# Kernel tuning notes

Measured on AMD Instinct MI355X. Metric: run time of the kernel, lower is better.

The kernel has to match this reference:

```python
import jax, jax.numpy as jnp
import numpy as np

B, NUM_CLASSES, H, W, CF = 2, 19, 64, 64, 256
TOPK_IDX = 20  # hard-coded in the torch source: sorted descending value at index 20


def _cosine(x):
    # x: [B, N, D] -> clamped cosine affinity [B, N, N]
    xn = x / (jnp.linalg.norm(x, axis=2, keepdims=True) + 1e-9)
    return jnp.maximum(jnp.einsum('bnd,bmd->bnm', xn, xn), 0.0)


def _conv1x1(x, w, b):
    # x: [B, C, H, W], w: [O, C], b: [O]
    return jnp.einsum('bchw,oc->bohw', x, w) + b[None, :, None, None]


def setup_inputs() -> dict:
    key = jax.random.key(0)
    ks = jax.random.split(key, 12)
    s_c = (2.0 / NUM_CLASSES) ** 0.5  # kaiming fan_in scale for 1x1 conv
    s_f = (2.0 / CF) ** 0.5
    return {
        'pred': jax.random.normal(ks[0], (B, NUM_CLASSES, H, W), jnp.float32),
        'feat': jax.random.normal(ks[1], (B, CF, H, W), jnp.float32),
        'w_cls1': jax.random.normal(ks[2], (NUM_CLASSES, NUM_CLASSES), jnp.float32) * s_c,
        'b_cls1': jnp.zeros((NUM_CLASSES,), jnp.float32),
        'w_cls2': jax.random.normal(ks[3], (NUM_CLASSES, NUM_CLASSES), jnp.float32) * s_c,
        'b_cls2': jnp.zeros((NUM_CLASSES,), jnp.float32),
        'w_pro1': jax.random.normal(ks[4], (CF, CF), jnp.float32) * s_f,
        'b_pro1': jnp.zeros((CF,), jnp.float32),
        'w_pro2': jax.random.normal(ks[5], (CF, CF), jnp.float32) * s_f,
        'b_pro2': jnp.zeros((CF,), jnp.float32),
        'class_weight': jnp.ones((NUM_CLASSES,), jnp.float32),
    }


def reference(pred, feat, w_cls1, b_cls1, w_cls2, b_cls2,
              w_pro1, b_pro1, w_pro2, b_pro2, class_weight):
    bsz, c, h, w = feat.shape
    C = pred.shape[1]
    N = h * w
    feat_flat = feat.reshape(bsz, c, N).transpose(0, 2, 1)  # [B, N, 256]

    # --- no_grad block 1: confidence mask + top-k sparsified cosine affinity ---
    prob = jax.nn.softmax(pred, axis=1)
    p_prob = prob.max(axis=1)      # [B, H, W]
    p_max = prob.argmax(axis=1)    # [B, H, W]
    cwm = class_weight / (class_weight.max() + 1e-10) * 0.95
    mask = ((p_prob >= 0.95) | (p_prob >= cwm[p_max])).astype(jnp.float32)
    mask = jax.lax.stop_gradient(mask.reshape(bsz, N, 1))  # broadcast over classes

    aff1 = _cosine(feat_flat)                                # [B, N, N]
    thr = -jnp.sort(-aff1, axis=-1)[:, :, TOPK_IDX:TOPK_IDX + 1]  # per-row 21st largest
    aff1 = jnp.where(aff1 < thr, 0.0, aff1)
    aff1 = jax.lax.stop_gradient(aff1 + aff1.transpose(0, 2, 1))

    # --- degree-normalized propagation of predictions ---
    pred_flat = pred.reshape(bsz, C, N).transpose(0, 2, 1)   # [B, N, C]
    d1 = (aff1.sum(-1) + 1e-10) ** -0.5                      # D^{-1/2}
    aff1n = d1[:, :, None] * aff1 * d1[:, None, :]           # D^{-1/2} A D^{-1/2}
    p2 = jnp.einsum('bnm,bmc->bnc', aff1n, pred_flat)
    p3 = (0.8 * p2 + 0.2 * pred_flat) * (1.0 - mask) + (0.2 * p2 + 0.8 * pred_flat) * mask
    pred2 = p3.transpose(0, 2, 1).reshape(bsz, C, h, w)
    pred_out = _conv1x1(_conv1x1(pred2, w_cls1, b_cls1), w_cls2, b_cls2)

    # --- no_grad block 2: class-consistency-masked affinity over refined softmax ---
    oh = jax.nn.one_hot(p_max, C, dtype=jnp.float32)         # [B, H, W, C]
    # faithful to torch: permute(0,2,3,1) on the already-[B,H,W,C] one-hot, then flat view
    oh = jnp.transpose(oh, (0, 2, 3, 1)).reshape(bsz, -1, C)
    sp = jax.nn.softmax(pred_out, axis=1).reshape(bsz, C, N).transpose(0, 2, 1)
    aff_f = _cosine(sp)
    aff_f = jnp.where(_cosine(oh) == 0.0, 0.0, aff_f)
    d2 = (aff_f.sum(-1) + 1e-10) ** -0.5
    aff_fn = jax.lax.stop_gradient(d2[:, :, None] * aff_f * d2[:, None, :])

    # --- propagate features and project ---
    new_feat = jnp.einsum('bnm,bmc->bnc', aff_fn, feat_flat)
    new_feat = new_feat.transpose(0, 2, 1).reshape(bsz, c, h, w)
    feat_out = _conv1x1(jax.nn.relu(_conv1x1(new_feat, w_pro1, b_pro1)), w_pro2, b_pro2)
    return pred_out, feat_out
```

## Files before the change

### kernel.cpp

```cpp
#include <hip/hip_runtime.h>

#define NN 4096
#define DD 256
#define CC 19
#define BB 2
#define KSPLIT 4

typedef __attribute__((ext_vector_type(8))) short bf16x8;
typedef _Float16 f16x8 __attribute__((ext_vector_type(8)));
typedef __attribute__((ext_vector_type(4))) float f32x4;

#define GLL16(gp, lp) __builtin_amdgcn_global_load_lds( \
    (const __attribute__((address_space(1))) unsigned int*)(gp), \
    (__attribute__((address_space(3))) unsigned int*)(lp), 16, 0, 0)

__device__ inline unsigned short f2b(float f) {
  unsigned int u = __float_as_uint(f);
  return (unsigned short)((u + 0x7FFFu + ((u >> 16) & 1u)) >> 16);
}
__device__ inline float b2f(unsigned short h) {
  return __uint_as_float(((unsigned int)h) << 16);
}
__device__ inline unsigned int pack2(float a, float b) {
  return (unsigned int)f2b(a) | ((unsigned int)f2b(b) << 16);
}
__device__ inline void split16(float x, unsigned short& h, unsigned short& l) {
  _Float16 hh = (_Float16)x;
  float hf = (float)hh;
  _Float16 ll = (_Float16)((x - hf) * 2048.0f);
  h = *reinterpret_cast<unsigned short*>(&hh);
  l = *reinterpret_cast<unsigned short*>(&ll);
}

__global__ __launch_bounds__(256) void k_prep(const float* __restrict__ pred,
                                              const float* __restrict__ cw,
                                              const float* __restrict__ feat,
                                              float* __restrict__ maskb,
                                              unsigned int* __restrict__ ohbits,
                                              unsigned short* __restrict__ xh,
                                              unsigned short* __restrict__ xl) {
  int g = blockIdx.x * 256 + threadIdx.x;
  int b = g >> 12, n = g & (NN - 1);
  {
    const float* p = pred + (size_t)b * CC * NN + n;
    float v[CC];
    float mx = -1e30f; int am = 0;
#pragma unroll
    for (int c = 0; c < CC; ++c) {
      float t = p[(size_t)c * NN];
      v[c] = t;
      if (t > mx) { mx = t; am = c; }
    }
    float s = 0.f;
#pragma unroll
    for (int c = 0; c < CC; ++c) s += expf(v[c] - mx);
    float pprob = 1.f / s;
    float cmax = 0.f;
#pragma unroll
    for (int c = 0; c < CC; ++c) cmax = fmaxf(cmax, cw[c]);
    float cwm = cw[am] / (cmax + 1e-10f) * 0.95f;
    maskb[g] = (pprob >= 0.95f || pprob >= cwm) ? 1.f : 0.f;
    int h = n >> 6, w = n & 63;
    int L = w * (CC * 64) + am * 64 + h;
    atomicOr(&ohbits[b * NN + L / CC], 1u << (L % CC));
  }
  {
    const float* f = feat + (size_t)b * DD * NN + n;
    float s = 0.f;
    for (int d = 0; d < DD; ++d) { float t = f[(size_t)d * NN]; s += t * t; }
    float r = 1.f / (sqrtf(s) + 1e-9f);
    size_t ob = ((size_t)b * NN + n) * DD;
    for (int d = 0; d < DD; d += 4) {
      ushort4 oh, ol;
      split16(f[(size_t)d * NN] * r, oh.x, ol.x);
      split16(f[(size_t)(d + 1) * NN] * r, oh.y, ol.y);
      split16(f[(size_t)(d + 2) * NN] * r, oh.z, ol.z);
      split16(f[(size_t)(d + 3) * NN] * r, oh.w, ol.w);
      *reinterpret_cast<ushort4*>(&xh[ob + d]) = oh;
      *reinterpret_cast<ushort4*>(&xl[ob + d]) = ol;
    }
  }
}

__global__ __launch_bounds__(256, 2) void k_gram1(const unsigned short* __restrict__ xh,
                                                  const unsigned short* __restrict__ xl,
                                                  float* __restrict__ M) {
  int L = blockIdx.x;
  int b = blockIdx.y;
  int I = 0;
  while (L >= 32 - I) { L -= 32 - I; ++I; }
  int J = I + L;
  int i0 = I * 128, j0 = J * 128;
  float* Mb = M + (size_t)b * NN * NN;
  const unsigned short* XH = xh + (size_t)b * NN * DD;
  const unsigned short* XL = xl + (size_t)b * NN * DD;
  __shared__ unsigned short stage[2][4][128][32];
  int t = threadIdx.x;
  int wave = t >> 6, lane = t & 63;
  int wr = (wave & 1) * 64, wc = (wave >> 1) * 64;
  int lrow = lane & 15, quad = lane >> 4;
  int sel = (lrow >> 1) & 3;
  f32x4 accH[4][4] = {}, accL[4][4] = {};
  const unsigned short* src = (wave == 0) ? XH + (size_t)i0 * DD
                             : (wave == 1) ? XL + (size_t)i0 * DD
                             : (wave == 2) ? XH + (size_t)j0 * DD
                                           : XL + (size_t)j0 * DD;
  int srow = lane >> 2;
  int spart = (lane & 3) ^ ((lane >> 3) & 3);
#pragma unroll
  for (int e = 0; e < 8; ++e)
    GLL16(&src[(size_t)(e * 16 + srow) * DD + spart * 8], &stage[0][wave][e * 16][0]);
  __syncthreads();
  int cur = 0;
  for (int k0 = 0; k0 < DD; k0 += 32) {
    if (k0 + 32 < DD) {
#pragma unroll
      for (int e = 0; e < 8; ++e)
        GLL16(&src[(size_t)(e * 16 + srow) * DD + k0 + 32 + spart * 8],
              &stage[cur ^ 1][wave][e * 16][0]);
    }
    f16x8 ah[4], al[4], bh[4], bl[4];
#pragma unroll
    for (int i = 0; i < 4; ++i) {
      int ra = wr + i * 16 + lrow;
      int rb = wc + i * 16 + lrow;
      int sl = (quad ^ sel) * 8;
      ah[i] = *reinterpret_cast<const f16x8*>(&stage[cur][0][ra][sl]);
      al[i] = *reinterpret_cast<const f16x8*>(&stage[cur][1][ra][sl]);
      bh[i] = *reinterpret_cast<const f16x8*>(&stage[cur][2][rb][sl]);
      bl[i] = *reinterpret_cast<const f16x8*>(&stage[cur][3][rb][sl]);
    }
#pragma unroll
    for (int i = 0; i < 4; ++i) {
#pragma unroll
      for (int j = 0; j < 4; ++j) {
        accH[i][j] = __builtin_amdgcn_mfma_f32_16x16x32_f16(ah[i], bh[j], accH[i][j], 0, 0, 0);
        accL[i][j] = __builtin_amdgcn_mfma_f32_16x16x32_f16(ah[i], bl[j], accL[i][j], 0, 0, 0);
        accL[i][j] = __builtin_amdgcn_mfma_f32_16x16x32_f16(al[i], bh[j], accL[i][j], 0, 0, 0);
      }
    }
    __syncthreads();
    cur ^= 1;
  }
#pragma unroll
  for (int i = 0; i < 4; ++i)
#pragma unroll
    for (int j = 0; j < 4; ++j)
#pragma unroll
      for (int reg = 0; reg < 4; ++reg)
        accH[i][j][reg] = fmaxf(accH[i][j][reg] + accL[i][j][reg] * 4.8828125e-4f, 0.f);
  float* buf = (float*)stage;
  int rr = t >> 4, cc = t & 15;
  for (int half = 0; half < 2; ++half) {
    __syncthreads();
    if ((wr >> 6) == half) {
#pragma unroll
      for (int i = 0; i < 4; ++i)
#pragma unroll
        for (int j = 0; j < 4; ++j)
#pragma unroll
          for (int reg = 0; reg < 4; ++reg)
            buf[(i * 16 + quad * 4 + reg) * 132 + wc + j * 16 + lrow] = accH[i][j][reg];
    }
    __syncthreads();
#pragma unroll
    for (int i = 0; i < 4; ++i) {
      int row = rr + i * 16;
#pragma unroll
      for (int q = 0; q < 2; ++q) {
        int col = cc * 4 + q * 64;
        *reinterpret_cast<float4*>(&Mb[(size_t)(i0 + half * 64 + row) * NN + j0 + col]) =
            *reinterpret_cast<float4*>(&buf[row * 132 + col]);
      }
    }
  }
  if (I != J) {
    for (int half = 0; half < 2; ++half) {
      __syncthreads();
      if ((wc >> 6) == half) {
#pragma unroll
        for (int i = 0; i < 4; ++i)
#pragma unroll
          for (int j = 0; j < 4; ++j)
#pragma unroll
            for (int reg = 0; reg < 4; ++reg)
              buf[(j * 16 + lrow) * 132 + wr + i * 16 + quad * 4 + reg] = accH[i][j][reg];
      }
      __syncthreads();
#pragma unroll
      for (int i = 0; i < 4; ++i) {
        int row = rr + i * 16;
#pragma unroll
        for (int q = 0; q < 2; ++q) {
          int col = cc * 4 + q * 64;
          *reinterpret_cast<float4*>(&Mb[(size_t)(j0 + half * 64 + row) * NN + i0 + col]) =
              *reinterpret_cast<float4*>(&buf[row * 132 + col]);
        }
      }
    }
  }
}

__global__ __launch_bounds__(256, 2) void k_topk(const float* __restrict__ M,
                                                 float* __restrict__ thr) {
  __shared__ unsigned int cbuf[4][64];
  int b = blockIdx.y;
  int wave = threadIdx.x >> 6, lane = threadIdx.x & 63;
  int n = blockIdx.x * 4 + wave;
  const float* row = M + (size_t)b * NN * NN + (size_t)n * NN;
  uint4 v[16];
#pragma unroll
  for (int e = 0; e < 16; ++e) {
    unsigned long long addr = (unsigned long long)(row + lane * 4 + e * 256);
    asm volatile("global_load_dwordx4 %0, %1, off" : "=v"(v[e]) : "v"(addr));
  }
  asm volatile("s_waitcnt vmcnt(0)" ::: "memory");
  __builtin_amdgcn_sched_barrier(0);
  unsigned int mx = 0u;
#pragma unroll
  for (int e = 0; e < 16; ++e) {
    unsigned int a = v[e].x > v[e].y ? v[e].x : v[e].y;
    unsigned int c2 = v[e].z > v[e].w ? v[e].z : v[e].w;
    a = a > c2 ? a : c2;
    mx = mx > a ? mx : a;
  }
  unsigned int lo = 0u, hi = 0x3FC00000u;
  while (lo < hi) {
    unsigned int mid = lo + ((hi - lo + 1) >> 1);
    if (__popcll(__ballot(mx >= mid)) >= 21) lo = mid; else hi = mid - 1;
  }
  unsigned int s = lo;
  unsigned int base = 0;
  unsigned long long ltmask = (1ull << lane) - 1ull;
#pragma unroll
  for (int e = 0; e < 16; ++e) {
#pragma unroll
    for (int q = 0; q < 4; ++q) {
      unsigned int val = (q == 0) ? v[e].x : (q == 1) ? v[e].y : (q == 2) ? v[e].z : v[e].w;
      unsigned long long mk = __ballot(val >= s);
      if (mk) {
        unsigned int pos = base + (unsigned int)__popcll(mk & ltmask);
        if (val >= s && pos < 64u) cbuf[wave][pos] = val;
        base += (unsigned int)__popcll(mk);
      }
    }
  }
  asm volatile("s_waitcnt lgkmcnt(0)" ::: "memory");
  __builtin_amdgcn_sched_barrier(0);
  unsigned int t = s;
  if (base <= 64u) {
    unsigned int cand = (lane < (int)base) ? cbuf[wave][lane] : 0u;
    lo = s; hi = 0x3FC00000u;
    while (lo < hi) {
      unsigned int mid = lo + ((hi - lo + 1) >> 1);
      if (__popcll(__ballot(cand >= mid)) >= 21) lo = mid; else hi = mid - 1;
    }
    t = lo;
  }
  {
    unsigned int t1 = t + 1u;
    int c1 = 0, c2 = 0;
#pragma unroll
    for (int e = 0; e < 16; ++e) {
      c1 += (int)__popcll(__ballot(v[e].x >= t));
      c1 += (int)__popcll(__ballot(v[e].y >= t));
      c1 += (int)__popcll(__ballot(v[e].z >= t));
      c1 += (int)__popcll(__ballot(v[e].w >= t));
      c2 += (int)__popcll(__ballot(v[e].x >= t1));
      c2 += (int)__popcll(__ballot(v[e].y >= t1));
      c2 += (int)__popcll(__ballot(v[e].z >= t1));
      c2 += (int)__popcll(__ballot(v[e].w >= t1));
    }
    if (!(c1 >= 21 && c2 < 21)) {
      lo = 0u; hi = 0x40000000u;
      while (lo < hi) {
        unsigned int mid = lo + ((hi - lo + 1) >> 1);
        int c = 0;
#pragma unroll
        for (int e = 0; e < 16; ++e) {
          c += (int)__popcll(__ballot(v[e].x >= mid));
          c += (int)__popcll(__ballot(v[e].y >= mid));
          c += (int)__popcll(__ballot(v[e].z >= mid));
          c += (int)__popcll(__ballot(v[e].w >= mid));
        }
        if (c >= 21) lo = mid; else hi = mid - 1;
      }
      t = lo;
    }
  }
  if (lane == 0) thr[b * NN + n] = __uint_as_float(t);
}

__global__ __launch_bounds__(256) void k_symm(float* __restrict__ M, const float* __restrict__ thr,
                                              float* __restrict__ dsum) {
  int L = blockIdx.x;
  int b = blockIdx.y;
  int I = 0;
  while (L >= 64 - I) { L -= 64 - I; ++I; }
  int J = I + L;
  float* Mb = M + (size_t)b * NN * NN;
  unsigned short* Mus = (unsigned short*)Mb;
  const float* th = thr + b * NN;
  __shared__ float A[64][65];
  int t = threadIdx.x;
  int i0 = I * 64, j0 = J * 64;
  float areg[16];
#pragma unroll
  for (int e = 0; e < 16; ++e) {
    int lin = t + e * 256;
    int i = lin >> 6, j = lin & 63;
    areg[e] = Mb[(size_t)(i0 + i) * NN + j0 + j];
  }
#pragma unroll
  for (int e = 0; e < 16; ++e) {
    int lin = t + e * 256;
    int i = lin >> 6, j = lin & 63;
    float a = areg[e];
    float v = a * ((a >= th[i0 + i] ? 1.f : 0.f) + (a >= th[j0 + j] ? 1.f : 0.f));
    A[i][j] = v;
  }
  __syncthreads();
  {
    int i = t >> 2, seg = (t & 3) * 16;
    float v[16];
#pragma unroll
    for (int q = 0; q < 4; ++q)
      *reinterpret_cast<float4*>(&v[q * 4]) = *reinterpret_cast<float4*>(&A[i][seg + q * 4]);
    unsigned int pk[8];
#pragma unroll
    for (int q = 0; q < 8; ++q) pk[q] = pack2(v[2 * q], v[2 * q + 1]);
    size_t ub = 2 * (size_t)(i0 + i) * NN + 2 * (size_t)j0 + seg;
    *reinterpret_cast<int4*>(&Mus[ub])     = *reinterpret_cast<int4*>(&pk[0]);
    *reinterpret_cast<int4*>(&Mus[ub + 8]) = *reinterpret_cast<int4*>(&pk[4]);
  }
  if (I != J) {
    int j = t >> 2, seg = (t & 3) * 16;
    float v[16];
#pragma unroll
    for (int e = 0; e < 16; ++e) v[e] = A[seg + e][j];
    unsigned int pk[8];
#pragma unroll
    for (int q = 0; q < 8; ++q) pk[q] = pack2(v[2 * q], v[2 * q + 1]);
    size_t ub = 2 * (size_t)(j0 + j) * NN + 2 * (size_t)i0 + seg;
    *reinterpret_cast<int4*>(&Mus[ub])     = *reinterpret_cast<int4*>(&pk[0]);
    *reinterpret_cast<int4*>(&Mus[ub + 8]) = *reinterpret_cast<int4*>(&pk[4]);
  }
  if (t < 64) {
    float s = 0.f;
#pragma unroll
    for (int j = 0; j < 64; ++j) s += A[t][j];
    atomicAdd(&dsum[b * NN + i0 + t], s);
  } else if (t < 128 && I != J) {
    int j = t - 64;
    float s = 0.f;
#pragma unroll
    for (int i = 0; i < 64; ++i) s += A[i][j];
    atomicAdd(&dsum[b * NN + j0 + j], s);
  }
}

__global__ void k_make_yb(const float* __restrict__ pred, const float* __restrict__ d1,
                          unsigned short* __restrict__ ybh) {
  int g = blockIdx.x * 256 + threadIdx.x;
  int idx = g * 4;
  int b = idx / (32 * NN);
  int c = (idx / NN) & 31;
  int n = idx & (NN - 1);
  ushort4 o = make_ushort4(0, 0, 0, 0);
  if (c < CC) {
    float4 p = *reinterpret_cast<const float4*>(&pred[((size_t)b * CC + c) * NN + n]);
    const float* dd = d1 + b * NN + n;
    o.x = f2b(p.x * (1.f / sqrtf(dd[0] + 1e-10f)));
    o.y = f2b(p.y * (1.f / sqrtf(dd[1] + 1e-10f)));
    o.z = f2b(p.z * (1.f / sqrtf(dd[2] + 1e-10f)));
    o.w = f2b(p.w * (1.f / sqrtf(dd[3] + 1e-10f)));
  }
  *reinterpret_cast<ushort4*>(&ybh[idx]) = o;
}

__global__ __launch_bounds__(256, 2) void k_p2_mfma(
    const float* __restrict__ M, const unsigned short* __restrict__ ybh,
    const float* __restrict__ d1, float* __restrict__ p2b) {
  int b = blockIdx.y;
  int n0 = blockIdx.x * 64;
  const unsigned short* Mus = (const unsigned short*)(M + (size_t)b * NN * NN);
  const unsigned short* Y = ybh + (size_t)b * 32 * NN;
  __shared__ unsigned short As2[2][64][64];
  __shared__ unsigned short Ys2[2][32][64];
  int t = threadIdx.x;
  int wave = t >> 6, lane = t & 63;
  int wn = (wave & 1) * 32;
  int wc = (wave >> 1) * 16;
  int lrow = lane & 15, quad = lane >> 4;
  f32x4 acc[2] = {{0.f,0.f,0.f,0.f},{0.f,0.f,0.f,0.f}};
  int lr3 = lane >> 3;
  int srow = wave * 8 + lr3;
  int spart = (lane & 7) ^ lr3;
#pragma unroll
  for (int e = 0; e < 2; ++e)
    GLL16(&Mus[2 * (size_t)(n0 + e * 32 + srow) * NN + spart * 8],
          &As2[0][e * 32 + wave * 8][0]);
  GLL16(&Y[(size_t)srow * NN + spart * 8], &Ys2[0][wave * 8][0]);
  __syncthreads();
  int cur = 0;
  for (int m0 = 0; m0 < NN; m0 += 64) {
    if (m0 + 64 < NN) {
#pragma unroll
      for (int e = 0; e < 2; ++e)
        GLL16(&Mus[2 * (size_t)(n0 + e * 32 + srow) * NN + 2 * (size_t)(m0 + 64) + spart * 8],
              &As2[cur ^ 1][e * 32 + wave * 8][0]);
      GLL16(&Y[(size_t)srow * NN + m0 + 64 + spart * 8], &Ys2[cur ^ 1][wave * 8][0]);
    }
#pragma unroll
    for (int kc = 0; kc < 2; ++kc) {
      int sl = ((kc * 4 + quad) ^ (lrow & 7)) * 8;
      bf16x8 bfr = *reinterpret_cast<const bf16x8*>(&Ys2[cur][wc + lrow][sl]);
#pragma unroll
      for (int i = 0; i < 2; ++i) {
        bf16x8 af = *reinterpret_cast<const bf16x8*>(&As2[cur][wn + i * 16 + lrow][sl]);
        acc[i] = __builtin_amdgcn_mfma_f32_16x16x32_bf16(af, bfr, acc[i], 0, 0, 0);
      }
    }
    __syncthreads();
    cur ^= 1;
  }
  int c = wc + lrow;
  if (c < CC) {
#pragma unroll
    for (int i = 0; i < 2; ++i) {
#pragma unroll
      for (int reg = 0; reg < 4; ++reg) {
        int n = n0 + wn + i * 16 + quad * 4 + reg;
        float dv = 1.f / sqrtf(d1[b * NN + n] + 1e-10f);
        p2b[((size_t)b * NN + n) * CC + c] = dv * acc[i][reg];
      }
    }
  }
}

__global__ __launch_bounds__(256) void k_pred_head(const float* __restrict__ pred,
    const float* __restrict__ p2b, const float* __restrict__ maskb,
    const float* __restrict__ w1, const float* __restrict__ b1,
    const float* __restrict__ w2, const float* __restrict__ b2,
    float* __restrict__ out, float* __restrict__ spnT) {
  __shared__ float sw1[CC * CC], sw2[CC * CC], sb1[CC], sb2[CC];
  int t = threadIdx.x;
  for (int i = t; i < CC * CC; i += 256) { sw1[i] = w1[i]; sw2[i] = w2[i]; }
  if (t < CC) { sb1[t] = b1[t]; sb2[t] = b2[t]; }
  __syncthreads();
  int g = blockIdx.x * 256 + t;
  int b = g >> 12, n = g & (NN - 1);
  float m = maskb[g];
  float ca = (m > 0.5f) ? 0.2f : 0.8f;
  float cb = (m > 0.5f) ? 0.8f : 0.2f;
  const float* P = pred + (size_t)b * CC * NN + n;
  const float* Q = p2b + (size_t)g * CC;
  float p3[CC];
#pragma unroll
  for (int c = 0; c < CC; ++c) p3[c] = ca * Q[c] + cb * P[(size_t)c * NN];
  float midv[CC];
#pragma unroll
  for (int o = 0; o < CC; ++o) {
    float s = sb1[o];
#pragma unroll
    for (int c = 0; c < CC; ++c) s += sw1[o * CC + c] * p3[c];
    midv[o] = s;
  }
  float ov[CC];
  float mx = -1e30f;
#pragma unroll
  for (int o = 0; o < CC; ++o) {
    float s = sb2[o];
#pragma unroll
    for (int c = 0; c < CC; ++c) s += sw2[o * CC + c] * midv[c];
    ov[o] = s;
    out[(size_t)b * CC * NN + (size_t)o * NN + n] = s;
    mx = fmaxf(mx, s);
  }
  float se = 0.f;
  float e[CC];
#pragma unroll
  for (int o = 0; o < CC; ++o) { e[o] = expf(ov[o] - mx); se += e[o]; }
  float inv = 1.f / se;
  float nrm = 0.f;
#pragma unroll
  for (int o = 0; o < CC; ++o) { float sp = e[o] * inv; e[o] = sp; nrm += sp * sp; }
  float rn = 1.f / (sqrtf(nrm) + 1e-9f);
#pragma unroll
  for (int o = 0; o < CC; ++o) spnT[(size_t)b * CC * NN + (size_t)o * NN + n] = e[o] * rn;
}

__global__ __launch_bounds__(256) void k_gram2(const float* __restrict__ spnT,
    const unsigned int* __restrict__ bits, unsigned short* __restrict__ Mh,
    float* __restrict__ d2) {
  int L = blockIdx.x;
  int b = blockIdx.y;
  int I = 0;
  while (L >= 64 - I) { L -= 64 - I; ++I; }
  int J = I + L;
  const float* X = spnT + (size_t)b * CC * NN;
  unsigned short* Mb = Mh + (size_t)b * NN * NN;
  __shared__ float sA[CC][64], sB[CC][64];
  __shared__ unsigned int bI[64], bJ[64];
  __shared__ float tr[64][65];
  int t = threadIdx.x;
  int r = t >> 4, c = t & 15;
  int i0 = I * 64, j0 = J * 64;
  for (int e = t; e < CC * 64; e += 256) {
    int k = e >> 6, col = e & 63;
    sA[k][col] = X[(size_t)k * NN + i0 + col];
    sB[k][col] = X[(size_t)k * NN + j0 + col];
  }
  if (t < 64) bI[t] = bits[b * NN + i0 + t];
  else if (t < 128) bJ[t - 64] = bits[b * NN + j0 + t - 64];
  __syncthreads();
  float acc[4][4] = {};
#pragma unroll
  for (int k = 0; k < CC; ++k) {
    float av[4], bv[4];
#pragma unroll
    for (int i = 0; i < 4; ++i) av[i] = sA[k][r * 4 + i];
#pragma unroll
    for (int j = 0; j < 4; ++j) bv[j] = sB[k][c * 4 + j];
#pragma unroll
    for (int i = 0; i < 4; ++i) {
#pragma unroll
      for (int j = 0; j < 4; ++j) acc[i][j] += av[i] * bv[j];
    }
  }
  float rs[4];
#pragma unroll
  for (int i = 0; i < 4; ++i) {
#pragma unroll
    for (int j = 0; j < 4; ++j) {
      bool keep = (bI[r * 4 + i] & bJ[c * 4 + j]) != 0u;
      acc[i][j] = keep ? fmaxf(acc[i][j], 0.f) : 0.f;
      acc[i][j] = b2f(f2b(acc[i][j]));
    }
    ushort4 v;
    v.x = f2b(acc[i][0]); v.y = f2b(acc[i][1]); v.z = f2b(acc[i][2]); v.w = f2b(acc[i][3]);
    *reinterpret_cast<ushort4*>(&Mb[(size_t)(i0 + r * 4 + i) * NN + j0 + c * 4]) = v;
    rs[i] = acc[i][0] + acc[i][1] + acc[i][2] + acc[i][3];
  }
#pragma unroll
  for (int m = 1; m < 16; m <<= 1) {
#pragma unroll
    for (int i = 0; i < 4; ++i) rs[i] += __shfl_xor(rs[i], m);
  }
  if ((t & 15) == 0) {
#pragma unroll
    for (int i = 0; i < 4; ++i) atomicAdd(&d2[b * NN + i0 + r * 4 + i], rs[i]);
  }
  if (I != J) {
#pragma unroll
    for (int i = 0; i < 4; ++i) {
#pragma unroll
      for (int j = 0; j < 4; ++j) tr[r * 4 + i][c * 4 + j] = acc[i][j];
    }
    __syncthreads();
#pragma unroll
    for (int e = 0; e < 16; ++e) {
      int lin = t + e * 256;
      int jr = lin >> 6, ic = lin & 63;
      Mb[(size_t)(j0 + jr) * NN + i0 + ic] = f2b(tr[ic][jr]);
    }
    if (t < 64) {
      float s = 0.f;
#pragma unroll
      for (int i = 0; i < 64; ++i) s += tr[i][t];
      atomicAdd(&d2[b * NN + j0 + t], s);
    }
  }
}

__global__ void k_make_z(const float* __restrict__ feat, const float* __restrict__ d2,
                         unsigned short* __restrict__ zb) {
  int g = blockIdx.x * 256 + threadIdx.x;
  int idx = g * 4;
  int b = idx / (DD * NN);
  int m = idx & (NN - 1);
  float4 f = *reinterpret_cast<const float4*>(&feat[idx]);
  const float* dd = d2 + b * NN + m;
  ushort4 o;
  o.x = f2b(f.x * (1.f / sqrtf(dd[0] + 1e-10f)));
  o.y = f2b(f.y * (1.f / sqrtf(dd[1] + 1e-10f)));
  o.z = f2b(f.z * (1.f / sqrtf(dd[2] + 1e-10f)));
  o.w = f2b(f.w * (1.f / sqrtf(dd[3] + 1e-10f)));
  *reinterpret_cast<ushort4*>(&zb[idx]) = o;
}

__global__ void k_prep_w(const float* __restrict__ w1, const float* __restrict__ w2,
                         unsigned short* __restrict__ wb1, unsigned short* __restrict__ wb2) {
  int g = blockIdx.x * 256 + threadIdx.x;
  wb1[g] = f2b(w1[g]);
  wb2[g] = f2b(w2[g]);
}

__global__ __launch_bounds__(256, 2) void k_newfeat_mfma(
    const unsigned short* __restrict__ Mh, const unsigned short* __restrict__ zb,
    float* __restrict__ nfp) {
  int zz = blockIdx.z;
  int b = zz / KSPLIT, ks = zz % KSPLIT;
  int nblk = blockIdx.x;
  int dblk = blockIdx.y;
  const int KLEN = NN / KSPLIT;
  const unsigned short* A = zb + (size_t)b * DD * NN + (size_t)(dblk * 64) * NN + ks * KLEN;
  const unsigned short* Bm = Mh + (size_t)b * NN * NN + (size_t)(nblk * 64) * NN + ks * KLEN;
  __shared__ unsigned short As[2][64][64];
  __shared__ unsigned short Bs[2][64][64];
  int t = threadIdx.x;
  int wave = t >> 6, lane = t & 63;
  int wd = (wave & 1) * 32, wn = (wave >> 1) * 32;
  int lrow = lane & 15, quad = lane >> 4;
  f32x4 acc[2][2] = {{{0.f,0.f,0.f,0.f},{0.f,0.f,0.f,0.f}},{{0.f,0.f,0.f,0.f},{0.f,0.f,0.f,0.f}}};
  int lr3 = lane >> 3;
  int srow = wave * 8 + lr3;
  int spart = (lane & 7) ^ lr3;
#pragma unroll
  for (int e = 0; e < 2; ++e) {
    GLL16(&A [(size_t)(e * 32 + srow) * NN + spart * 8], &As[0][e * 32 + wave * 8][0]);
    GLL16(&Bm[(size_t)(e * 32 + srow) * NN + spart * 8], &Bs[0][e * 32 + wave * 8][0]);
  }
  __syncthreads();
  int cur = 0;
  for (int m0 = 0; m0 < KLEN; m0 += 64) {
    if (m0 + 64 < KLEN) {
#pragma unroll
      for (int e = 0; e < 2; ++e) {
        GLL16(&A [(size_t)(e * 32 + srow) * NN + m0 + 64 + spart * 8],
              &As[cur ^ 1][e * 32 + wave * 8][0]);
        GLL16(&Bm[(size_t)(e * 32 + srow) * NN + m0 + 64 + spart * 8],
              &Bs[cur ^ 1][e * 32 + wave * 8][0]);
      }
    }
#pragma unroll
    for (int kc = 0; kc < 2; ++kc) {
      int sl = ((kc * 4 + quad) ^ (lrow & 7)) * 8;
      bf16x8 af[2], bfr[2];
#pragma unroll
      for (int i = 0; i < 2; ++i) {
        af[i]  = *reinterpret_cast<const bf16x8*>(&As[cur][wd + i * 16 + lrow][sl]);
        bfr[i] = *reinterpret_cast<const bf16x8*>(&Bs[cur][wn + i * 16 + lrow][sl]);
      }
#pragma unroll
      for (int i = 0; i < 2; ++i)
#pragma unroll
        for (int j = 0; j < 2; ++j)
          acc[i][j] = __builtin_amdgcn_mfma_f32_16x16x32_bf16(af[i], bfr[j], acc[i][j], 0, 0, 0);
    }
    __syncthreads();
    cur ^= 1;
  }
#pragma unroll
  for (int j = 0; j < 2; ++j) {
    int n = nblk * 64 + wn + j * 16 + lrow;
#pragma unroll
    for (int i = 0; i < 2; ++i) {
      int d = dblk * 64 + wd + i * 16 + quad * 4;
      float4 v = make_float4(acc[i][j].x, acc[i][j].y, acc[i][j].z, acc[i][j].w);
      *reinterpret_cast<float4*>(&nfp[((size_t)zz * NN + n) * DD + d]) = v;
    }
  }
}

__global__ void k_nf_reduce(const float* __restrict__ nfp, const float* __restrict__ d2,
                            unsigned short* __restrict__ nfh) {
  int g = blockIdx.x * 256 + threadIdx.x;
  int idx = g * 4;
  int b = idx / (NN * DD);
  int n = (idx / DD) & (NN - 1);
  size_t base = (size_t)idx + (size_t)b * (KSPLIT - 1) * NN * DD;
  float4 s = make_float4(0.f, 0.f, 0.f, 0.f);
#pragma unroll
  for (int ks = 0; ks < KSPLIT; ++ks) {
    float4 v = *reinterpret_cast<const float4*>(&nfp[base + (size_t)ks * NN * DD]);
    s.x += v.x; s.y += v.y; s.z += v.z; s.w += v.w;
  }
  float sc = 1.f / sqrtf(d2[b * NN + n] + 1e-10f);
  ushort4 o;
  o.x = f2b(s.x * sc); o.y = f2b(s.y * sc); o.z = f2b(s.z * sc); o.w = f2b(s.w * sc);
  *reinterpret_cast<ushort4*>(&nfh[idx]) = o;
}

__global__ __launch_bounds__(256) void k_conv1_mfma(
    const unsigned short* __restrict__ nfh, const unsigned short* __restrict__ wb1,
    const float* __restrict__ b1, unsigned short* __restrict__ midh) {
  int b = blockIdx.z;
  int nblk = blockIdx.x;
  int oblk = blockIdx.y;
  int n0 = nblk * 64, o0 = oblk * 64;
  __shared__ unsigned short As[64][72];
  __shared__ unsigned short Bs[64][72];
  int t = threadIdx.x;
  int wave = t >> 6, lane = t & 63;
  int wn = (wave & 1) * 32, wo = (wave >> 1) * 32;
  int lrow = lane & 15, quad = lane >> 4;
  f32x4 acc[2][2] = {{{0.f,0.f,0.f,0.f},{0.f,0.f,0.f,0.f}},{{0.f,0.f,0.f,0.f},{0.f,0.f,0.f,0.f}}};
  int sr = t >> 3, sc = (t & 7) * 8;
  for (int d0 = 0; d0 < DD; d0 += 64) {
#pragma unroll
    for (int e = 0; e < 2; ++e) {
      int rr = sr + e * 32;
      *reinterpret_cast<int4*>(&As[rr][sc]) =
          *reinterpret_cast<const int4*>(&nfh[((size_t)b * NN + n0 + rr) * DD + d0 + sc]);
      *reinterpret_cast<int4*>(&Bs[rr][sc]) =
          *reinterpret_cast<const int4*>(&wb1[(size_t)(o0 + rr) * DD + d0 + sc]);
    }
    __syncthreads();
#pragma unroll
    for (int kc = 0; kc < 2; ++kc) {
      int ko = kc * 32 + quad * 8;
      bf16x8 af[2], bfr[2];
#pragma unroll
      for (int i = 0; i < 2; ++i) {
        af[i]  = *reinterpret_cast<const bf16x8*>(&As[wn + i * 16 + lrow][ko]);
        bfr[i] = *reinterpret_cast<const bf16x8*>(&Bs[wo + i * 16 + lrow][ko]);
      }
#pragma unroll
      for (int i = 0; i < 2; ++i)
#pragma unroll
        for (int j = 0; j < 2; ++j)
          acc[i][j] = __builtin_amdgcn_mfma_f32_16x16x32_bf16(af[i], bfr[j], acc[i][j], 0, 0, 0);
    }
    __syncthreads();
  }
#pragma unroll
  for (int j = 0; j < 2; ++j) {
    int o = o0 + wo + j * 16 + lrow;
    float bias = b1[o];
#pragma unroll
    for (int i = 0; i < 2; ++i) {
      int nb = n0 + wn + i * 16 + quad * 4;
      ushort4 v;
      v.x = f2b(fmaxf(acc[i][j].x + bias, 0.f));
      v.y = f2b(fmaxf(acc[i][j].y + bias, 0.f));
      v.z = f2b(fmaxf(acc[i][j].z + bias, 0.f));
      v.w = f2b(fmaxf(acc[i][j].w + bias, 0.f));
      *reinterpret_cast<ushort4*>(&midh[((size_t)b * DD + o) * NN + nb]) = v;
    }
  }
}

__global__ __launch_bounds__(256) void k_conv2_mfma(
    const unsigned short* __restrict__ midh, const unsigned short* __restrict__ wb2,
    const float* __restrict__ b2, float* __restrict__ outp) {
  int b = blockIdx.z;
  int nblk = blockIdx.x;
  int oblk = blockIdx.y;
  int n0 = nblk * 64, o0 = oblk * 64;
  __shared__ unsigned short As[64][72];
  __shared__ unsigned short Bs[64][72];
  int t = threadIdx.x;
  int wave = t >> 6, lane = t & 63;
  int wn = (wave & 1) * 32, wo = (wave >> 1) * 32;
  int lrow = lane & 15, quad = lane >> 4;
  f32x4 acc[2][2] = {{{0.f,0.f,0.f,0.f},{0.f,0.f,0.f,0.f}},{{0.f,0.f,0.f,0.f},{0.f,0.f,0.f,0.f}}};
  int sr = t >> 3, sc = (t & 7) * 8;
  for (int d0 = 0; d0 < DD; d0 += 64) {
#pragma unroll
    for (int e = 0; e < 2; ++e) {
      int rr = sr + e * 32;
      *reinterpret_cast<int4*>(&Bs[rr][sc]) =
          *reinterpret_cast<const int4*>(&wb2[(size_t)(o0 + rr) * DD + d0 + sc]);
      unsigned short v[8];
      *reinterpret_cast<int4*>(v) =
          *reinterpret_cast<const int4*>(&midh[((size_t)b * DD + d0 + rr) * NN + n0 + sc]);
#pragma unroll
      for (int j = 0; j < 8; ++j) As[sc + j][rr] = v[j];
    }
    __syncthreads();
#pragma unroll
    for (int kc = 0; kc < 2; ++kc) {
      int ko = kc * 32 + quad * 8;
      bf16x8 af[2], bfr[2];
#pragma unroll
      for (int i = 0; i < 2; ++i) {
        af[i]  = *reinterpret_cast<const bf16x8*>(&As[wn + i * 16 + lrow][ko]);
        bfr[i] = *reinterpret_cast<const bf16x8*>(&Bs[wo + i * 16 + lrow][ko]);
      }
#pragma unroll
      for (int i = 0; i < 2; ++i)
#pragma unroll
        for (int j = 0; j < 2; ++j)
          acc[i][j] = __builtin_amdgcn_mfma_f32_16x16x32_bf16(af[i], bfr[j], acc[i][j], 0, 0, 0);
    }
    __syncthreads();
  }
#pragma unroll
  for (int j = 0; j < 2; ++j) {
    int o = o0 + wo + j * 16 + lrow;
    float bias = b2[o];
#pragma unroll
    for (int i = 0; i < 2; ++i) {
      int nb = n0 + wn + i * 16 + quad * 4;
      float4 v = make_float4(acc[i][j].x + bias, acc[i][j].y + bias,
                             acc[i][j].z + bias, acc[i][j].w + bias);
      *reinterpret_cast<float4*>(&outp[((size_t)b * DD + o) * NN + nb]) = v;
    }
  }
}

extern "C" void kernel_launch(void* const* d_in, const int* in_sizes, int n_in,
                              void* d_out, int out_size, void* d_ws, size_t ws_size,
                              hipStream_t stream) {
  (void)in_sizes; (void)n_in; (void)out_size; (void)ws_size;
  const float* pred   = (const float*)d_in[0];
  const float* feat   = (const float*)d_in[1];
  const float* w_cls1 = (const float*)d_in[2];
  const float* b_cls1 = (const float*)d_in[3];
  const float* w_cls2 = (const float*)d_in[4];
  const float* b_cls2 = (const float*)d_in[5];
  const float* w_pro1 = (const float*)d_in[6];
  const float* b_pro1 = (const float*)d_in[7];
  const float* w_pro2 = (const float*)d_in[8];
  const float* b_pro2 = (const float*)d_in[9];
  const float* cw     = (const float*)d_in[10];
  float* out = (float*)d_out;

  float* Mbuf = (float*)d_ws;
  float* spnT = Mbuf + (size_t)BB * NN * NN;
  float* p2b  = spnT + (size_t)BB * CC * NN;
  float* thr  = p2b + (size_t)BB * NN * CC;
  float* dsum = thr + BB * NN;
  float* d2s  = dsum + BB * NN;
  float* maskb = d2s + BB * NN;
  unsigned int* ohbits = (unsigned int*)(maskb + BB * NN);
  unsigned short* xh   = (unsigned short*)(ohbits + BB * NN);
  unsigned short* xl   = xh + (size_t)BB * NN * DD;
  unsigned short* nfh  = xl + (size_t)BB * NN * DD;
  unsigned short* midh = nfh + (size_t)BB * NN * DD;
  unsigned short* zb   = midh + (size_t)BB * DD * NN;
  unsigned short* wb1  = zb + (size_t)BB * DD * NN;
  unsigned short* wb2  = wb1 + (size_t)DD * DD;
  unsigned short* ybh  = wb2 + (size_t)DD * DD;
  unsigned short* Mh   = (unsigned short*)Mbuf;
  float* nfp = (float*)(Mh + (size_t)BB * NN * NN);

  hipMemsetAsync(dsum, 0, sizeof(float) * 2 * BB * NN, stream);
  hipMemsetAsync(ohbits, 0, sizeof(unsigned int) * BB * NN, stream);

  k_prep<<<BB * NN / 256, 256, 0, stream>>>(pred, cw, feat, maskb, ohbits, xh, xl);
  k_gram1<<<dim3(528, BB), 256, 0, stream>>>(xh, xl, Mbuf);
  k_topk<<<dim3(NN / 4, BB), 256, 0, stream>>>(Mbuf, thr);
  k_symm<<<dim3(2080, BB), 256, 0, stream>>>(Mbuf, thr, dsum);
  k_make_yb<<<BB * 32 * NN / 4 / 256, 256, 0, stream>>>(pred, dsum, ybh);
  k_p2_mfma<<<dim3(NN / 64, BB), 256, 0, stream>>>(Mbuf, ybh, dsum, p2b);
  k_pred_head<<<BB * NN / 256, 256, 0, stream>>>(pred, p2b, maskb, w_cls1, b_cls1,
                                                 w_cls2, b_cls2, out, spnT);
  k_gram2<<<dim3(2080, BB), 256, 0, stream>>>(spnT, ohbits, Mh, d2s);
  k_make_z<<<BB * DD * NN / 4 / 256, 256, 0, stream>>>(feat, d2s, zb);
  k_prep_w<<<DD * DD / 256, 256, 0, stream>>>(w_pro1, w_pro2, wb1, wb2);
  k_newfeat_mfma<<<dim3(64, 4, BB * KSPLIT), 256, 0, stream>>>(Mh, zb, nfp);
  k_nf_reduce<<<BB * NN * DD / 4 / 256, 256, 0, stream>>>(nfp, d2s, nfh);
  k_conv1_mfma<<<dim3(64, 4, BB), 256, 0, stream>>>(nfh, wb1, b_pro1, midh);
  k_conv2_mfma<<<dim3(64, 4, BB), 256, 0, stream>>>(midh, wb2, b_pro2,
                                                    out + (size_t)BB * CC * NN);
}
```

Before: 372.0 us.

## Compute second affinity Gram with bf16 MFMA from packed padded softmax rows

The pred head now writes the normalized softmax as bf16 rows padded to 32 channels instead of fp32 channel-major. The second Gram kernel loads those rows straight into LDS with global_load_lds and computes the 64x64 tile with 16x16x32 bf16 MFMA, replacing the scalar FMA loop. It stages the masked result in a bf16 LDS tile so the direct tile is written with wide row stores, and it takes row and column sums from that tile. Rounding the inputs to bf16 changes the affinity values slightly compared with the fp32 dot products.

New measurement: 332.4 us. -10.7%, faster.

```diff
diff --git a/kernel.cpp b/kernel.cpp
--- a/kernel.cpp
+++ b/kernel.cpp
@@ -442,7 +442,7 @@
     const float* __restrict__ p2b, const float* __restrict__ maskb,
     const float* __restrict__ w1, const float* __restrict__ b1,
     const float* __restrict__ w2, const float* __restrict__ b2,
-    float* __restrict__ out, float* __restrict__ spnT) {
+    float* __restrict__ out, unsigned short* __restrict__ spnP) {
   __shared__ float sw1[CC * CC], sw2[CC * CC], sb1[CC], sb2[CC];
   int t = threadIdx.x;
   for (int i = t; i < CC * CC; i += 256) { sw1[i] = w1[i]; sw2[i] = w2[i]; }
@@ -486,11 +486,18 @@
 #pragma unroll
   for (int o = 0; o < CC; ++o) { float sp = e[o] * inv; e[o] = sp; nrm += sp * sp; }
   float rn = 1.f / (sqrtf(nrm) + 1e-9f);
-#pragma unroll
-  for (int o = 0; o < CC; ++o) spnT[(size_t)b * CC * NN + (size_t)o * NN + n] = e[o] * rn;
-}
-
-__global__ __launch_bounds__(256) void k_gram2(const float* __restrict__ spnT,
+  unsigned short sp[32];
+#pragma unroll
+  for (int o = 0; o < CC; ++o) sp[o] = f2b(e[o] * rn);
+#pragma unroll
+  for (int o = CC; o < 32; ++o) sp[o] = 0;
+  unsigned short* dst = spnP + (size_t)g * 32;
+#pragma unroll
+  for (int q = 0; q < 4; ++q)
+    *reinterpret_cast<int4*>(&dst[q * 8]) = *reinterpret_cast<int4*>(&sp[q * 8]);
+}
+
+__global__ __launch_bounds__(256) void k_gram2(const unsigned short* __restrict__ spnP,
     const unsigned int* __restrict__ bits, unsigned short* __restrict__ Mh,
     float* __restrict__ d2) {
   int L = blockIdx.x;
@@ -498,78 +505,81 @@
   int I = 0;
   while (L >= 64 - I) { L -= 64 - I; ++I; }
   int J = I + L;
-  const float* X = spnT + (size_t)b * CC * NN;
+  const unsigned short* X = spnP + (size_t)b * NN * 32;
   unsigned short* Mb = Mh + (size_t)b * NN * NN;
-  __shared__ float sA[CC][64], sB[CC][64];
+  __shared__ unsigned short As[64][32], Bs[64][32];
+  __shared__ unsigned short tr[64][66];
   __shared__ unsigned int bI[64], bJ[64];
-  __shared__ float tr[64][65];
   int t = threadIdx.x;
-  int r = t >> 4, c = t & 15;
+  int wave = t >> 6, lane = t & 63;
+  int lrow = lane & 15, quad = lane >> 4;
   int i0 = I * 64, j0 = J * 64;
-  for (int e = t; e < CC * 64; e += 256) {
-    int k = e >> 6, col = e & 63;
-    sA[k][col] = X[(size_t)k * NN + i0 + col];
-    sB[k][col] = X[(size_t)k * NN + j0 + col];
-  }
+  int srow = wave * 16 + (lane >> 2);
+  int spart = (lane & 3) ^ ((lane >> 3) & 3);
+  GLL16(&X[(size_t)(i0 + srow) * 32 + spart * 8], &As[wave * 16][0]);
+  GLL16(&X[(size_t)(j0 + srow) * 32 + spart * 8], &Bs[wave * 16][0]);
   if (t < 64) bI[t] = bits[b * NN + i0 + t];
   else if (t < 128) bJ[t - 64] = bits[b * NN + j0 + t - 64];
   __syncthreads();
-  float acc[4][4] = {};
-#pragma unroll
-  for (int k = 0; k < CC; ++k) {
-    float av[4], bv[4];
-#pragma unroll
-    for (int i = 0; i < 4; ++i) av[i] = sA[k][r * 4 + i];
-#pragma unroll
-    for (int j = 0; j < 4; ++j) bv[j] = sB[k][c * 4 + j];
-#pragma unroll
-    for (int i = 0; i < 4; ++i) {
-#pragma unroll
-      for (int j = 0; j < 4; ++j) acc[i][j] += av[i] * bv[j];
-    }
-  }
-  float rs[4];
-#pragma unroll
-  for (int i = 0; i < 4; ++i) {
-#pragma unroll
-    for (int j = 0; j < 4; ++j) {
-      bool keep = (bI[r * 4 + i] & bJ[c * 4 + j]) != 0u;
-      acc[i][j] = keep ? fmaxf(acc[i][j], 0.f) : 0.f;
-      acc[i][j] = b2f(f2b(acc[i][j]));
-    }
-    ushort4 v;
-    v.x = f2b(acc[i][0]); v.y = f2b(acc[i][1]); v.z = f2b(acc[i][2]); v.w = f2b(acc[i][3]);
-    *reinterpret_cast<ushort4*>(&Mb[(size_t)(i0 + r * 4 + i) * NN + j0 + c * 4]) = v;
-    rs[i] = acc[i][0] + acc[i][1] + acc[i][2] + acc[i][3];
-  }
-#pragma unroll
-  for (int m = 1; m < 16; m <<= 1) {
-#pragma unroll
-    for (int i = 0; i < 4; ++i) rs[i] += __shfl_xor(rs[i], m);
-  }
-  if ((t & 15) == 0) {
-#pragma unroll
-    for (int i = 0; i < 4; ++i) atomicAdd(&d2[b * NN + i0 + r * 4 + i], rs[i]);
+  int wi = wave & 1, wj = wave >> 1;
+  int sl = (quad ^ ((lrow >> 1) & 3)) * 8;
+  bf16x8 af[2], bfr[2];
+#pragma unroll
+  for (int i = 0; i < 2; ++i) {
+    af[i]  = *reinterpret_cast<const bf16x8*>(&As[wi * 32 + i * 16 + lrow][sl]);
+    bfr[i] = *reinterpret_cast<const bf16x8*>(&Bs[wj * 32 + i * 16 + lrow][sl]);
+  }
+  f32x4 acc[2][2] = {{{0.f,0.f,0.f,0.f},{0.f,0.f,0.f,0.f}},{{0.f,0.f,0.f,0.f},{0.f,0.f,0.f,0.f}}};
+#pragma unroll
+  for (int i = 0; i < 2; ++i)
+#pragma unroll
+    for (int j = 0; j < 2; ++j)
+      acc[i][j] = __builtin_amdgcn_mfma_f32_16x16x32_bf16(af[i], bfr[j], acc[i][j], 0, 0, 0);
+#pragma unroll
+  for (int i = 0; i < 2; ++i) {
+#pragma unroll
+    for (int j = 0; j < 2; ++j) {
+#pragma unroll
+      for (int reg = 0; reg < 4; ++reg) {
+        int row = wi * 32 + i * 16 + quad * 4 + reg;
+        int col = wj * 32 + j * 16 + lrow;
+        bool keep = (bI[row] & bJ[col]) != 0u;
+        float v = keep ? fmaxf(acc[i][j][reg], 0.f) : 0.f;
+        tr[row][col] = f2b(v);
+      }
+    }
+  }
+  __syncthreads();
+  {
+    int row = t >> 2, seg = (t & 3) * 16;
+    unsigned int w[8];
+#pragma unroll
+    for (int k = 0; k < 8; ++k)
+      w[k] = *reinterpret_cast<const unsigned int*>(&tr[row][seg + 2 * k]);
+    *reinterpret_cast<int4*>(&Mb[(size_t)(i0 + row) * NN + j0 + seg])     =
+        *reinterpret_cast<int4*>(&w[0]);
+    *reinterpret_cast<int4*>(&Mb[(size_t)(i0 + row) * NN + j0 + seg + 8]) =
+        *reinterpret_cast<int4*>(&w[4]);
   }
   if (I != J) {
-#pragma unroll
-    for (int i = 0; i < 4; ++i) {
-#pragma unroll
-      for (int j = 0; j < 4; ++j) tr[r * 4 + i][c * 4 + j] = acc[i][j];
-    }
-    __syncthreads();
 #pragma unroll
     for (int e = 0; e < 16; ++e) {
       int lin = t + e * 256;
       int jr = lin >> 6, ic = lin & 63;
-      Mb[(size_t)(j0 + jr) * NN + i0 + ic] = f2b(tr[ic][jr]);
-    }
-    if (t < 64) {
-      float s = 0.f;
-#pragma unroll
-      for (int i = 0; i < 64; ++i) s += tr[i][t];
-      atomicAdd(&d2[b * NN + j0 + t], s);
-    }
+      Mb[(size_t)(j0 + jr) * NN + i0 + ic] = tr[ic][jr];
+    }
+  }
+  if (t < 64) {
+    float s = 0.f;
+#pragma unroll
+    for (int c = 0; c < 64; ++c) s += b2f(tr[t][c]);
+    atomicAdd(&d2[b * NN + i0 + t], s);
+  } else if (t < 128 && I != J) {
+    int c = t - 64;
+    float s = 0.f;
+#pragma unroll
+    for (int i = 0; i < 64; ++i) s += b2f(tr[i][c]);
+    atomicAdd(&d2[b * NN + j0 + c], s);
   }
 }
 
@@ -834,6 +844,7 @@
   unsigned short* wb2  = wb1 + (size_t)DD * DD;
   unsigned short* ybh  = wb2 + (size_t)DD * DD;
   unsigned short* Mh   = (unsigned short*)Mbuf;
+  unsigned short* spnP = (unsigned short*)spnT;
   float* nfp = (float*)(Mh + (size_t)BB * NN * NN);
 
   hipMemsetAsync(dsum, 0, sizeof(float) * 2 * BB * NN, stream);
@@ -846,8 +857,8 @@
   k_make_yb<<<BB * 32 * NN / 4 / 256, 256, 0, stream>>>(pred, dsum, ybh);
   k_p2_mfma<<<dim3(NN / 64, BB), 256, 0, stream>>>(Mbuf, ybh, dsum, p2b);
   k_pred_head<<<BB * NN / 256, 256, 0, stream>>>(pred, p2b, maskb, w_cls1, b_cls1,
-                                                 w_cls2, b_cls2, out, spnT);
-  k_gram2<<<dim3(2080, BB), 256, 0, stream>>>(spnT, ohbits, Mh, d2s);
+                                                 w_cls2, b_cls2, out, spnP);
+  k_gram2<<<dim3(2080, BB), 256, 0, stream>>>(spnP, ohbits, Mh, d2s);
   k_make_z<<<BB * DD * NN / 4 / 256, 256, 0, stream>>>(feat, d2s, zb);
   k_prep_w<<<DD * DD / 256, 256, 0, stream>>>(w_pro1, w_pro2, wb1, wb2);
   k_newfeat_mfma<<<dim3(64, 4, BB * KSPLIT), 256, 0, stream>>>(Mh, zb, nfp);
```
